# Kernel optimization log

Measured on AMD Instinct MI355X. Metric: run time of the kernel, lower is better.

The kernel has to match this reference:

```python
import jax, jax.numpy as jnp
import numpy as np

N, E = 100000, 1600000
D_IN, D_HID, D_OUT = 128, 64, 64
NEG_SLOPE = 0.2


def setup_inputs() -> dict:
    key = jax.random.key(0)
    ks = jax.random.split(key, 12)
    x = jax.random.normal(ks[0], (N, D_IN), dtype=jnp.float32)
    edge_index = jax.random.randint(ks[1], (2, E), 0, N, dtype=jnp.int64)
    edge_attr = jax.random.normal(ks[2], (E, 8), dtype=jnp.float32)
    s1 = 1.0 / np.sqrt(D_IN)
    s2 = 1.0 / np.sqrt(D_HID)
    return {
        "x": x,
        "edge_index": edge_index,
        "edge_attr": edge_attr,
        "W1": jax.random.normal(ks[3], (D_IN, D_HID), dtype=jnp.float32) * s1,
        "att_src1": jax.random.normal(ks[4], (D_HID,), dtype=jnp.float32) * s2,
        "att_dst1": jax.random.normal(ks[5], (D_HID,), dtype=jnp.float32) * s2,
        "b1": jnp.zeros((D_HID,), dtype=jnp.float32),
        "W2": jax.random.normal(ks[6], (D_HID, D_OUT), dtype=jnp.float32) * s2,
        "att_src2": jax.random.normal(ks[7], (D_OUT,), dtype=jnp.float32) * (1.0 / np.sqrt(D_OUT)),
        "att_dst2": jax.random.normal(ks[8], (D_OUT,), dtype=jnp.float32) * (1.0 / np.sqrt(D_OUT)),
        "b2": jnp.zeros((D_OUT,), dtype=jnp.float32),
    }


def gat_conv(x, src, dst, W, att_src, att_dst, b, n_nodes):
    # h = W x  (single head)
    h = x @ W                                   # [N, F]
    a_src = h @ att_src                         # [N]
    a_dst = h @ att_dst                         # [N]
    e = jax.nn.leaky_relu(a_src[src] + a_dst[dst], NEG_SLOPE)  # [E]
    # softmax over incoming edges per target node (numerically stable)
    e_max = jax.ops.segment_max(e, dst, num_segments=n_nodes)
    w = jnp.exp(e - e_max[dst])
    denom = jax.ops.segment_sum(w, dst, num_segments=n_nodes)
    alpha = w / (denom[dst] + 1e-16)            # [E]
    out = jax.ops.segment_sum(h[src] * alpha[:, None], dst, num_segments=n_nodes)
    return out + b


def reference(x, edge_index, edge_attr, W1, att_src1, att_dst1, b1, W2, att_src2, att_dst2, b2):
    n_nodes = x.shape[0]
    # PyG GATConv default: add self-loops; edge_attr unused (edge_dim=None)
    loops = jnp.arange(n_nodes, dtype=edge_index.dtype)
    src = jnp.concatenate([edge_index[0], loops])
    dst = jnp.concatenate([edge_index[1], loops])
    h = gat_conv(x, src, dst, W1, att_src1, att_dst1, b1, n_nodes)
    h = jax.nn.relu(h)
    h = gat_conv(h, src, dst, W2, att_src2, att_dst2, b2, n_nodes)
    # global_mean_pool with batch=None -> mean over all nodes, shape [1, D_OUT]
    return jnp.mean(h, axis=0, keepdims=True)
```

## Files before the change

### kernel.cpp

```cpp
#include <hip/hip_runtime.h>
#include <hip/hip_bf16.h>
#include <cstdint>

#define NEG_SLOPE 0.2f
#define SCAN_ELEMS 1024
#define BUCKET_SHIFT 9
#define CHUNK 2048

typedef __attribute__((ext_vector_type(4))) int            i32x4;
typedef __attribute__((ext_vector_type(4))) float          f32x4;
typedef __attribute__((ext_vector_type(8))) unsigned short u16x8;
typedef __attribute__((ext_vector_type(4))) unsigned short u16x4;

__device__ inline unsigned short f2bf(float f) {
    unsigned xi = __float_as_uint(f);
    unsigned r = xi + 0x7fffu + ((xi >> 16) & 1u);
    return (unsigned short)(r >> 16);
}
__device__ inline float bflo(unsigned g) { return __uint_as_float(g << 16); }
__device__ inline float bfhi(unsigned g) { return __uint_as_float(g & 0xffff0000u); }

__device__ inline int get_ei(const int* ei, int is64, long idx) {
    return is64 ? ei[2 * idx] : ei[(int)idx];
}

__device__ inline int detect_is64(const int* __restrict__ ei, int tid) {
    __shared__ int dred[4];
    int v = 0;
    for (int i = tid; i < 2048; i += 256) v |= ei[2 * i + 1];
#pragma unroll
    for (int off = 32; off; off >>= 1) v |= __shfl_xor(v, off);
    if ((tid & 63) == 0) dred[tid >> 6] = v;
    __syncthreads();
    int r = dred[0] | dred[1] | dred[2] | dred[3];
    __syncthreads();
    return (r == 0) ? 1 : 0;
}

__global__ __launch_bounds__(256) void p1_hist(const int* __restrict__ ei,
                                               int* __restrict__ HH,
                                               int E, int n, int nblk) {
    __shared__ int cnt[256];
    int tid = threadIdx.x;
    int is64 = detect_is64(ei, tid);
    int nbuk = (n + (1 << BUCKET_SHIFT) - 1) >> BUCKET_SHIFT;
    for (int b = tid; b < nbuk; b += 256) cnt[b] = 0;
    __syncthreads();
    int total = E + n;
    int beg = blockIdx.x * CHUNK;
    int end = beg + CHUNK; if (end > total) end = total;
    for (int i = beg + tid; i < end; i += 256) {
        int d = (i < E) ? get_ei(ei, is64, (long)E + i) : (i - E);
        atomicAdd(&cnt[d >> BUCKET_SHIFT], 1);
    }
    __syncthreads();
    for (int b = tid; b < nbuk; b += 256) HH[b * nblk + blockIdx.x] = cnt[b];
}

__global__ __launch_bounds__(256) void scan1_kernel(const int* __restrict__ src,
                                                    int* __restrict__ bsums, int n) {
    int t = threadIdx.x;
    int i0 = blockIdx.x * SCAN_ELEMS + 4 * t;
    int4 v = make_int4(0, 0, 0, 0);
    if (i0 + 3 < n) v = *(const int4*)(src + i0);
    else {
        if (i0 + 0 < n) v.x = src[i0 + 0];
        if (i0 + 1 < n) v.y = src[i0 + 1];
        if (i0 + 2 < n) v.z = src[i0 + 2];
        if (i0 + 3 < n) v.w = src[i0 + 3];
    }
    int s = v.x + v.y + v.z + v.w;
#pragma unroll
    for (int off = 32; off; off >>= 1) s += __shfl_down(s, off);
    __shared__ int ws[4];
    if ((t & 63) == 0) ws[t >> 6] = s;
    __syncthreads();
    if (t == 0) bsums[blockIdx.x] = ws[0] + ws[1] + ws[2] + ws[3];
}

__global__ __launch_bounds__(256) void scan3g_kernel(const int* __restrict__ src,
                                                     const int* __restrict__ bsums,
                                                     int* __restrict__ out, int n, int nb) {
    int b = blockIdx.x;
    int t = threadIdx.x;
    __shared__ int sb[256];
    int bv = (t < nb) ? bsums[t] : 0;
    sb[t] = bv;
    __syncthreads();
    for (int off = 1; off < 256; off <<= 1) {
        int u = (t >= off) ? sb[t - off] : 0;
        __syncthreads();
        sb[t] += u;
        __syncthreads();
    }
    int blockbase = (b == 0) ? 0 : sb[b - 1];

    int i0 = b * SCAN_ELEMS + 4 * t;
    int4 v = make_int4(0, 0, 0, 0);
    if (i0 + 3 < n) v = *(const int4*)(src + i0);
    else {
        if (i0 + 0 < n) v.x = src[i0 + 0];
        if (i0 + 1 < n) v.y = src[i0 + 1];
        if (i0 + 2 < n) v.z = src[i0 + 2];
        if (i0 + 3 < n) v.w = src[i0 + 3];
    }
    int s0 = v.x, s1 = s0 + v.y, s2 = s1 + v.z, s3 = s2 + v.w;
    __shared__ int sh[256];
    sh[t] = s3;
    __syncthreads();
    for (int off = 1; off < 256; off <<= 1) {
        int u = (t >= off) ? sh[t - off] : 0;
        __syncthreads();
        sh[t] += u;
        __syncthreads();
    }
    int base = blockbase + sh[t] - s3;
    if (i0 + 0 < n) out[i0 + 0] = base;
    if (i0 + 1 < n) out[i0 + 1] = base + s0;
    if (i0 + 2 < n) out[i0 + 2] = base + s1;
    if (i0 + 3 < n) out[i0 + 3] = base + s2;
}

__global__ __launch_bounds__(256) void p3_scatter(const int* __restrict__ ei,
                                                  const int* __restrict__ scanHH,
                                                  int* __restrict__ sorted,
                                                  int E, int n, int nblk) {
    __shared__ int base[256];
    __shared__ int cur[256];
    int tid = threadIdx.x;
    int is64 = detect_is64(ei, tid);
    int nbuk = (n + (1 << BUCKET_SHIFT) - 1) >> BUCKET_SHIFT;
    for (int b = tid; b < nbuk; b += 256) {
        base[b] = scanHH[b * nblk + blockIdx.x];
        cur[b] = 0;
    }
    __syncthreads();
    int total = E + n;
    int beg = blockIdx.x * CHUNK;
    int end = beg + CHUNK; if (end > total) end = total;
    for (int i = beg + tid; i < end; i += 256) {
        int s, d;
        if (i < E) {
            s = get_ei(ei, is64, i);
            d = get_ei(ei, is64, (long)E + i);
        } else {
            s = d = i - E;
        }
        int b = d >> BUCKET_SHIFT;
        int p = base[b] + atomicAdd(&cur[b], 1);
        sorted[p] = (s << BUCKET_SHIFT) | (d & ((1 << BUCKET_SHIFT) - 1));
    }
}

__global__ __launch_bounds__(256) void p4_finalize(const int* __restrict__ scanHH,
                                                   const int* __restrict__ sorted,
                                                   int* __restrict__ ptr,
                                                   int* __restrict__ csr_src,
                                                   int n, int nblk, int T) {
    int b = blockIdx.x;
    int nbuk = gridDim.x;
    int tid = threadIdx.x;
    int node0 = b << BUCKET_SHIFT;
    int nn = n - node0; if (nn > (1 << BUCKET_SHIFT)) nn = 1 << BUCKET_SHIFT;
    int beg = scanHH[b * nblk];
    int end = (b + 1 < nbuk) ? scanHH[(b + 1) * nblk] : T;

    __shared__ int cnt[512];
    __shared__ int pair[256];
    __shared__ int exc[512];
    cnt[tid] = 0; cnt[tid + 256] = 0;
    __syncthreads();
    for (int j = beg + tid; j < end; j += 256) {
        int v = sorted[j];
        atomicAdd(&cnt[v & ((1 << BUCKET_SHIFT) - 1)], 1);
    }
    __syncthreads();
    int psum = cnt[2 * tid] + cnt[2 * tid + 1];
    pair[tid] = psum;
    __syncthreads();
    for (int off = 1; off < 256; off <<= 1) {
        int u = (tid >= off) ? pair[tid - off] : 0;
        __syncthreads();
        pair[tid] += u;
        __syncthreads();
    }
    int pexc = pair[tid] - psum;
    exc[2 * tid] = pexc;
    exc[2 * tid + 1] = pexc + cnt[2 * tid];
    __syncthreads();
    for (int i = tid; i < nn; i += 256) ptr[node0 + i] = beg + exc[i];
    if (node0 + nn == n && tid == 0) ptr[n] = T;
    cnt[tid] = exc[tid]; cnt[tid + 256] = exc[tid + 256];
    __syncthreads();
    for (int j = beg + tid; j < end; j += 256) {
        int v = sorted[j];
        int p = beg + atomicAdd(&cnt[v & ((1 << BUCKET_SHIFT) - 1)], 1);
        csr_src[p] = ((unsigned)v) >> BUCKET_SHIFT;
    }
}

__global__ __launch_bounds__(256) void pack_w(const float* __restrict__ W1,
                                              const float* __restrict__ W2,
                                              unsigned short* __restrict__ wp1,
                                              unsigned short* __restrict__ wp2) {
    int t = blockIdx.x * 256 + threadIdx.x;
    if (t >= 24 * 64) return;
    int f = t >> 6, l = t & 63;
    int lm = l & 15, lg = l >> 4;
    const float* W = (f < 16) ? W1 : W2;
    unsigned short* wp = (f < 16) ? wp1 : wp2;
    int idx = (f < 16) ? f : (f - 16);
    int kt = idx >> 2, ct = idx & 3;
    union { u16x8 v; unsigned short u[8]; } o;
#pragma unroll
    for (int e = 0; e < 8; ++e)
        o.u[e] = f2bf(W[(size_t)(32 * kt + 8 * lg + e) * 64 + 16 * ct + lm]);
    *(u16x8*)(wp + ((size_t)idx * 64 + l) * 8) = o.v;
}

#define MFMA_BF16(acc, a, b) \
    asm("s_nop 1\n\tv_mfma_f32_16x16x32_bf16 %0, %1, %2, %0" \
        : "+v"(acc) : "v"(a), "v"(b))

template <int KT, bool XBF>
__global__ __launch_bounds__(256) void proj_mfma(const void* __restrict__ xin,
                                                 const unsigned short* __restrict__ Wp,
                                                 const float* __restrict__ att_s,
                                                 const float* __restrict__ att_d,
                                                 unsigned short* __restrict__ h2,
                                                 float* __restrict__ asrc,
                                                 float* __restrict__ adst, int n) {
    constexpr int K = 32 * KT;
    __shared__ alignas(16) unsigned short lb[4][16 * 72];
    int tid = threadIdx.x;
    int wid = tid >> 6, l = tid & 63;
    int lm = l & 15, lg = l >> 4;

    int node0 = blockIdx.x * 64 + wid * 16;
    if (node0 >= n) return;

    float as_c[4], ad_c[4];
#pragma unroll
    for (int ct = 0; ct < 4; ++ct) {
        as_c[ct] = att_s[16 * ct + lm];
        ad_c[ct] = att_d[16 * ct + lm];
    }

    f32x4 acc[4] = {};

    int arow = node0 + lm;
    bool rowok = arow < n;

#pragma unroll
    for (int kt = 0; kt < KT; ++kt) {
        i32x4 af = {0, 0, 0, 0};
        if (XBF) {
            const unsigned short* xb = (const unsigned short*)xin
                                       + (size_t)arow * K + 32 * kt + 8 * lg;
            if (rowok) af = *(const i32x4*)xb;
        } else {
            const float* xp = (const float*)xin + (size_t)arow * K + 8 * lg + 32 * kt;
            float4 v0 = make_float4(0.f, 0.f, 0.f, 0.f);
            float4 v1 = v0;
            if (rowok) {
                v0 = *(const float4*)(xp);
                v1 = *(const float4*)(xp + 4);
            }
            af[0] = (int)((unsigned)f2bf(v0.x) | ((unsigned)f2bf(v0.y) << 16));
            af[1] = (int)((unsigned)f2bf(v0.z) | ((unsigned)f2bf(v0.w) << 16));
            af[2] = (int)((unsigned)f2bf(v1.x) | ((unsigned)f2bf(v1.y) << 16));
            af[3] = (int)((unsigned)f2bf(v1.z) | ((unsigned)f2bf(v1.w) << 16));
        }
#pragma unroll
        for (int ct = 0; ct < 4; ++ct) {
            i32x4 bf = *(const i32x4*)(Wp + (((kt * 4 + ct) * 64) + l) * 8);
            MFMA_BF16(acc[ct], af, bf);
        }
    }
    asm volatile("s_nop 7\n\ts_nop 7"
                 : "+v"(acc[0]), "+v"(acc[1]), "+v"(acc[2]), "+v"(acc[3]));

    float ps[4], pd[4];
#pragma unroll
    for (int r = 0; r < 4; ++r) {
        float s = 0.f, d = 0.f;
#pragma unroll
        for (int ct = 0; ct < 4; ++ct) {
            s = fmaf(acc[ct][r], as_c[ct], s);
            d = fmaf(acc[ct][r], ad_c[ct], d);
        }
        ps[r] = s; pd[r] = d;
    }
#pragma unroll
    for (int off = 1; off < 16; off <<= 1) {
#pragma unroll
        for (int r = 0; r < 4; ++r) {
            ps[r] += __shfl_xor(ps[r], off);
            pd[r] += __shfl_xor(pd[r], off);
        }
    }
    if (lm == 0) {
#pragma unroll
        for (int r = 0; r < 4; ++r) {
            int node = node0 + 4 * lg + r;
            if (node < n) { asrc[node] = ps[r]; adst[node] = pd[r]; }
        }
    }

    unsigned short* wb = lb[wid];
#pragma unroll
    for (int ct = 0; ct < 4; ++ct)
#pragma unroll
        for (int r = 0; r < 4; ++r)
            wb[(4 * lg + r) * 72 + 16 * ct + lm] = f2bf(acc[ct][r]);
    asm volatile("s_waitcnt lgkmcnt(0)" ::: "memory");
    int ch = l & 7;
#pragma unroll
    for (int p = 0; p < 2; ++p) {
        int rr = (l >> 3) + 8 * p;
        u16x8 ov = *(const u16x8*)(wb + rr * 72 + 8 * ch);
        int onode = node0 + rr;
        if (onode < n)
            *(u16x8*)(h2 + (size_t)onode * 64 + 8 * ch) = ov;
    }
}

template <bool FMEAN>
__global__ __launch_bounds__(256) void agg_kernel(const int* __restrict__ ptr,
                                                  const int* __restrict__ srcs,
                                                  const unsigned short* __restrict__ h2,
                                                  const float* __restrict__ asrc,
                                                  const float* __restrict__ adst,
                                                  const float* __restrict__ bias,
                                                  unsigned short* __restrict__ outbf,
                                                  float* __restrict__ partials,
                                                  int n, int do_relu) {
    __shared__ int2  sm[4][64];
    __shared__ float red[256];
    int tid = threadIdx.x;
    int lane = tid & 63, wid = tid >> 6;
    int slot = lane >> 4, f = lane & 15;
    const char* h2b = (const char*)h2;
    unsigned fo = (unsigned)f << 3;
    float4 bv = *(const float4*)(bias + 4 * f);
    float ms0 = 0.f, ms1 = 0.f, ms2 = 0.f, ms3 = 0.f;

    int gwave = (blockIdx.x * blockDim.x + tid) >> 6;
    int nwaves = (gridDim.x * blockDim.x) >> 6;
    for (int node = gwave; node < n; node += nwaves) {
        int beg = ptr[node], end = ptr[node + 1];
        float ad = adst[node];
        float a0 = 0.f, a1 = 0.f, a2 = 0.f, a3 = 0.f, wsum = 0.f;
        for (int b = beg; b < end; b += 64) {
            int blen = end - b; if (blen > 64) blen = 64;
            int sv = 0; float wv = 0.f;
            if (lane < blen) {
                sv = srcs[b + lane];
                float e = asrc[sv] + ad;
                e = (e > 0.f) ? e : NEG_SLOPE * e;
                wv = __expf(e);
            }
            wsum += wv;
            sm[wid][lane] = make_int2(sv, __float_as_int(wv));
            int ni = (blen + 15) >> 4;
            for (int j = 0; j < ni; ++j) {
                int2 swv[4];
#pragma unroll
                for (int u = 0; u < 4; ++u)
                    swv[u] = sm[wid][16 * j + 4 * u + slot];
                uint2 g[4]; float w[4];
#pragma unroll
                for (int u = 0; u < 4; ++u) {
                    w[u] = __int_as_float(swv[u].y);
                    g[u] = *(const uint2*)(h2b + (((unsigned)swv[u].x << 7) + fo));
                }
#pragma unroll
                for (int u = 0; u < 4; ++u) {
                    a0 = fmaf(w[u], bflo(g[u].x), a0);
                    a1 = fmaf(w[u], bfhi(g[u].x), a1);
                    a2 = fmaf(w[u], bflo(g[u].y), a2);
                    a3 = fmaf(w[u], bfhi(g[u].y), a3);
                }
            }
        }
        a0 += __shfl_xor(a0, 16); a0 += __shfl_xor(a0, 32);
        a1 += __shfl_xor(a1, 16); a1 += __shfl_xor(a1, 32);
        a2 += __shfl_xor(a2, 16); a2 += __shfl_xor(a2, 32);
        a3 += __shfl_xor(a3, 16); a3 += __shfl_xor(a3, 32);
#pragma unroll
        for (int off = 32; off; off >>= 1) wsum += __shfl_xor(wsum, off);
        float inv = 1.f / (wsum + 1e-16f);
        float o0 = a0 * inv + bv.x;
        float o1 = a1 * inv + bv.y;
        float o2 = a2 * inv + bv.z;
        float o3 = a3 * inv + bv.w;
        if (!FMEAN) {
            if (do_relu) {
                o0 = fmaxf(o0, 0.f); o1 = fmaxf(o1, 0.f);
                o2 = fmaxf(o2, 0.f); o3 = fmaxf(o3, 0.f);
            }
            if (slot == 0) {
                u16x4 ov;
                ov[0] = f2bf(o0); ov[1] = f2bf(o1);
                ov[2] = f2bf(o2); ov[3] = f2bf(o3);
                *(u16x4*)(outbf + (size_t)node * 64 + 4 * f) = ov;
            }
        } else {
            if (slot == 0) { ms0 += o0; ms1 += o1; ms2 += o2; ms3 += o3; }
        }
    }
    if (FMEAN) {
        if (slot == 0)
            *(float4*)(red + wid * 64 + 4 * f) = make_float4(ms0, ms1, ms2, ms3);
        __syncthreads();
        if (tid < 64) {
            float t = red[tid] + red[64 + tid] + red[128 + tid] + red[192 + tid];
            partials[(size_t)blockIdx.x * 64 + tid] = t;
        }
    }
}

__global__ __launch_bounds__(256) void reduce_mean(const float* __restrict__ partials,
                                                   float* __restrict__ out,
                                                   int nb, float inv_n) {
    __shared__ float red[256];
    int f = threadIdx.x & 63;
    int w = threadIdx.x >> 6;
    int idx = blockIdx.x * 4 + w;
    int stride = gridDim.x * 4;
    float s = 0.f;
    for (int r = idx; r < nb; r += stride) s += partials[(size_t)r * 64 + f];
    red[threadIdx.x] = s;
    __syncthreads();
    if (w == 0) {
        float t = red[f] + red[64 + f] + red[128 + f] + red[192 + f];
        atomicAdd(&out[f], t * inv_n);
    }
}

extern "C" void kernel_launch(void* const* d_in, const int* in_sizes, int n_in,
                              void* d_out, int out_size, void* d_ws, size_t ws_size,
                              hipStream_t stream) {
    const float* x   = (const float*)d_in[0];
    const int*   ei  = (const int*)d_in[1];
    const float* W1  = (const float*)d_in[3];
    const float* as1 = (const float*)d_in[4];
    const float* ad1 = (const float*)d_in[5];
    const float* b1  = (const float*)d_in[6];
    const float* W2  = (const float*)d_in[7];
    const float* as2 = (const float*)d_in[8];
    const float* ad2 = (const float*)d_in[9];
    const float* b2  = (const float*)d_in[10];
    float* out = (float*)d_out;

    const int N = in_sizes[0] / 128;
    const int E = in_sizes[1] / 2;
    const int T = E + N;

    const int NBUK = (N + (1 << BUCKET_SHIFT) - 1) >> BUCKET_SHIFT;
    const int NBLK = (T + CHUNK - 1) / CHUNK;
    const int NHH  = NBUK * NBLK;
    const int NBS  = (NHH + SCAN_ELEMS - 1) / SCAN_ELEMS;
    const int AGRID = (N + 3) / 4;

    size_t off = 0;
    char* base = (char*)d_ws;
    auto alloc = [&](size_t bytes) -> void* {
        void* p = base + off;
        off += (bytes + 255) & ~(size_t)255;
        return p;
    };
    int*   ptr     = (int*)alloc(((size_t)N + 1) * 4);
    int*   bsums   = (int*)alloc(256 * 4);
    int*   HH      = (int*)alloc((size_t)NHH * 4);
    int*   scanHH  = (int*)alloc((size_t)NHH * 4);
    int*   csr_src = (int*)alloc((size_t)T * 4);
    float* asrc    = (float*)alloc((size_t)N * 4);
    float* adst    = (float*)alloc((size_t)N * 4);
    unsigned short* h2 = (unsigned short*)alloc((size_t)N * 64 * 2);
    unsigned short* bufB = (unsigned short*)alloc((size_t)N * 64 * 4);
    unsigned short* wp1 = (unsigned short*)alloc(16 * 64 * 8 * 2);
    unsigned short* wp2 = (unsigned short*)alloc(8 * 64 * 8 * 2);
    int*   sorted  = (int*)bufB;
    float* partials = (float*)bufB;
    (void)ws_size;

    pack_w<<<6, 256, 0, stream>>>(W1, W2, wp1, wp2);

    p1_hist<<<NBLK, 256, 0, stream>>>(ei, HH, E, N, NBLK);
    scan1_kernel<<<NBS, 256, 0, stream>>>(HH, bsums, NHH);
    scan3g_kernel<<<NBS, 256, 0, stream>>>(HH, bsums, scanHH, NHH, NBS);
    p3_scatter<<<NBLK, 256, 0, stream>>>(ei, scanHH, sorted, E, N, NBLK);
    p4_finalize<<<NBUK, 256, 0, stream>>>(scanHH, sorted, ptr, csr_src, N, NBLK, T);

    const int PGRID = (N + 63) / 64;

    proj_mfma<4, false><<<PGRID, 256, 0, stream>>>(x, wp1, as1, ad1, h2, asrc, adst, N);
    agg_kernel<false><<<AGRID, 256, 0, stream>>>(ptr, csr_src, h2, asrc, adst,
                                                 b1, bufB, nullptr, N, 1);

    proj_mfma<2, true><<<PGRID, 256, 0, stream>>>(bufB, wp2, as2, ad2, h2, asrc, adst, N);
    agg_kernel<true><<<AGRID, 256, 0, stream>>>(ptr, csr_src, h2, asrc, adst,
                                                b2, nullptr, partials, N, 0);
    hipMemsetAsync(out, 0, 64 * 4, stream);
    reduce_mean<<<64, 256, 0, stream>>>(partials, out, AGRID, 1.f / (float)N);
}
```

Baseline: 335.4 us.

## Restructure CSR build with global bucket counters and fuse histogram into projection

Replaces the per-block histogram matrix and two-pass scan with a single global bucket-count array filled by atomics. The histogram pass is fused into the first projection kernel. The scatter now stashes each chunk in LDS and reserves its bucket ranges with one atomic per bucket. It also doubles the gather unroll in aggregation, fixes the aggregation grid at 2048 blocks, and replaces the memset plus multi-block atomic reduction with a single-block reduction. Fewer launches and less scan work come at the cost of global atomic contention and a nondeterministic order within buckets.

```diff
diff --git a/kernel.cpp b/kernel.cpp
--- a/kernel.cpp
+++ b/kernel.cpp
@@ -3,9 +3,8 @@
 #include <cstdint>
 
 #define NEG_SLOPE 0.2f
-#define SCAN_ELEMS 1024
 #define BUCKET_SHIFT 9
-#define CHUNK 2048
+#define CHUNK 4096
 
 typedef __attribute__((ext_vector_type(4))) int            i32x4;
 typedef __attribute__((ext_vector_type(4))) float          f32x4;
@@ -37,185 +36,24 @@
     return (r == 0) ? 1 : 0;
 }
 
-__global__ __launch_bounds__(256) void p1_hist(const int* __restrict__ ei,
-                                               int* __restrict__ HH,
-                                               int E, int n, int nblk) {
+__device__ void p1_body(const int* __restrict__ ei, int* __restrict__ BT,
+                        int E, int n, int bid) {
     __shared__ int cnt[256];
     int tid = threadIdx.x;
     int is64 = detect_is64(ei, tid);
-    int nbuk = (n + (1 << BUCKET_SHIFT) - 1) >> BUCKET_SHIFT;
+    int nbuk = (n + 511) >> BUCKET_SHIFT;
     for (int b = tid; b < nbuk; b += 256) cnt[b] = 0;
     __syncthreads();
     int total = E + n;
-    int beg = blockIdx.x * CHUNK;
+    int beg = bid * CHUNK;
     int end = beg + CHUNK; if (end > total) end = total;
     for (int i = beg + tid; i < end; i += 256) {
         int d = (i < E) ? get_ei(ei, is64, (long)E + i) : (i - E);
         atomicAdd(&cnt[d >> BUCKET_SHIFT], 1);
     }
     __syncthreads();
-    for (int b = tid; b < nbuk; b += 256) HH[b * nblk + blockIdx.x] = cnt[b];
-}
-
-__global__ __launch_bounds__(256) void scan1_kernel(const int* __restrict__ src,
-                                                    int* __restrict__ bsums, int n) {
-    int t = threadIdx.x;
-    int i0 = blockIdx.x * SCAN_ELEMS + 4 * t;
-    int4 v = make_int4(0, 0, 0, 0);
-    if (i0 + 3 < n) v = *(const int4*)(src + i0);
-    else {
-        if (i0 + 0 < n) v.x = src[i0 + 0];
-        if (i0 + 1 < n) v.y = src[i0 + 1];
-        if (i0 + 2 < n) v.z = src[i0 + 2];
-        if (i0 + 3 < n) v.w = src[i0 + 3];
-    }
-    int s = v.x + v.y + v.z + v.w;
-#pragma unroll
-    for (int off = 32; off; off >>= 1) s += __shfl_down(s, off);
-    __shared__ int ws[4];
-    if ((t & 63) == 0) ws[t >> 6] = s;
-    __syncthreads();
-    if (t == 0) bsums[blockIdx.x] = ws[0] + ws[1] + ws[2] + ws[3];
-}
-
-__global__ __launch_bounds__(256) void scan3g_kernel(const int* __restrict__ src,
-                                                     const int* __restrict__ bsums,
-                                                     int* __restrict__ out, int n, int nb) {
-    int b = blockIdx.x;
-    int t = threadIdx.x;
-    __shared__ int sb[256];
-    int bv = (t < nb) ? bsums[t] : 0;
-    sb[t] = bv;
-    __syncthreads();
-    for (int off = 1; off < 256; off <<= 1) {
-        int u = (t >= off) ? sb[t - off] : 0;
-        __syncthreads();
-        sb[t] += u;
-        __syncthreads();
-    }
-    int blockbase = (b == 0) ? 0 : sb[b - 1];
-
-    int i0 = b * SCAN_ELEMS + 4 * t;
-    int4 v = make_int4(0, 0, 0, 0);
-    if (i0 + 3 < n) v = *(const int4*)(src + i0);
-    else {
-        if (i0 + 0 < n) v.x = src[i0 + 0];
-        if (i0 + 1 < n) v.y = src[i0 + 1];
-        if (i0 + 2 < n) v.z = src[i0 + 2];
-        if (i0 + 3 < n) v.w = src[i0 + 3];
-    }
-    int s0 = v.x, s1 = s0 + v.y, s2 = s1 + v.z, s3 = s2 + v.w;
-    __shared__ int sh[256];
-    sh[t] = s3;
-    __syncthreads();
-    for (int off = 1; off < 256; off <<= 1) {
-        int u = (t >= off) ? sh[t - off] : 0;
-        __syncthreads();
-        sh[t] += u;
-        __syncthreads();
-    }
-    int base = blockbase + sh[t] - s3;
-    if (i0 + 0 < n) out[i0 + 0] = base;
-    if (i0 + 1 < n) out[i0 + 1] = base + s0;
-    if (i0 + 2 < n) out[i0 + 2] = base + s1;
-    if (i0 + 3 < n) out[i0 + 3] = base + s2;
-}
-
-__global__ __launch_bounds__(256) void p3_scatter(const int* __restrict__ ei,
-                                                  const int* __restrict__ scanHH,
-                                                  int* __restrict__ sorted,
-                                                  int E, int n, int nblk) {
-    __shared__ int base[256];
-    __shared__ int cur[256];
-    int tid = threadIdx.x;
-    int is64 = detect_is64(ei, tid);
-    int nbuk = (n + (1 << BUCKET_SHIFT) - 1) >> BUCKET_SHIFT;
-    for (int b = tid; b < nbuk; b += 256) {
-        base[b] = scanHH[b * nblk + blockIdx.x];
-        cur[b] = 0;
-    }
-    __syncthreads();
-    int total = E + n;
-    int beg = blockIdx.x * CHUNK;
-    int end = beg + CHUNK; if (end > total) end = total;
-    for (int i = beg + tid; i < end; i += 256) {
-        int s, d;
-        if (i < E) {
-            s = get_ei(ei, is64, i);
-            d = get_ei(ei, is64, (long)E + i);
-        } else {
-            s = d = i - E;
-        }
-        int b = d >> BUCKET_SHIFT;
-        int p = base[b] + atomicAdd(&cur[b], 1);
-        sorted[p] = (s << BUCKET_SHIFT) | (d & ((1 << BUCKET_SHIFT) - 1));
-    }
-}
-
-__global__ __launch_bounds__(256) void p4_finalize(const int* __restrict__ scanHH,
-                                                   const int* __restrict__ sorted,
-                                                   int* __restrict__ ptr,
-                                                   int* __restrict__ csr_src,
-                                                   int n, int nblk, int T) {
-    int b = blockIdx.x;
-    int nbuk = gridDim.x;
-    int tid = threadIdx.x;
-    int node0 = b << BUCKET_SHIFT;
-    int nn = n - node0; if (nn > (1 << BUCKET_SHIFT)) nn = 1 << BUCKET_SHIFT;
-    int beg = scanHH[b * nblk];
-    int end = (b + 1 < nbuk) ? scanHH[(b + 1) * nblk] : T;
-
-    __shared__ int cnt[512];
-    __shared__ int pair[256];
-    __shared__ int exc[512];
-    cnt[tid] = 0; cnt[tid + 256] = 0;
-    __syncthreads();
-    for (int j = beg + tid; j < end; j += 256) {
-        int v = sorted[j];
-        atomicAdd(&cnt[v & ((1 << BUCKET_SHIFT) - 1)], 1);
-    }
-    __syncthreads();
-    int psum = cnt[2 * tid] + cnt[2 * tid + 1];
-    pair[tid] = psum;
-    __syncthreads();
-    for (int off = 1; off < 256; off <<= 1) {
-        int u = (tid >= off) ? pair[tid - off] : 0;
-        __syncthreads();
-        pair[tid] += u;
-        __syncthreads();
-    }
-    int pexc = pair[tid] - psum;
-    exc[2 * tid] = pexc;
-    exc[2 * tid + 1] = pexc + cnt[2 * tid];
-    __syncthreads();
-    for (int i = tid; i < nn; i += 256) ptr[node0 + i] = beg + exc[i];
-    if (node0 + nn == n && tid == 0) ptr[n] = T;
-    cnt[tid] = exc[tid]; cnt[tid + 256] = exc[tid + 256];
-    __syncthreads();
-    for (int j = beg + tid; j < end; j += 256) {
-        int v = sorted[j];
-        int p = beg + atomicAdd(&cnt[v & ((1 << BUCKET_SHIFT) - 1)], 1);
-        csr_src[p] = ((unsigned)v) >> BUCKET_SHIFT;
-    }
-}
-
-__global__ __launch_bounds__(256) void pack_w(const float* __restrict__ W1,
-                                              const float* __restrict__ W2,
-                                              unsigned short* __restrict__ wp1,
-                                              unsigned short* __restrict__ wp2) {
-    int t = blockIdx.x * 256 + threadIdx.x;
-    if (t >= 24 * 64) return;
-    int f = t >> 6, l = t & 63;
-    int lm = l & 15, lg = l >> 4;
-    const float* W = (f < 16) ? W1 : W2;
-    unsigned short* wp = (f < 16) ? wp1 : wp2;
-    int idx = (f < 16) ? f : (f - 16);
-    int kt = idx >> 2, ct = idx & 3;
-    union { u16x8 v; unsigned short u[8]; } o;
-#pragma unroll
-    for (int e = 0; e < 8; ++e)
-        o.u[e] = f2bf(W[(size_t)(32 * kt + 8 * lg + e) * 64 + 16 * ct + lm]);
-    *(u16x8*)(wp + ((size_t)idx * 64 + l) * 8) = o.v;
+    for (int b = tid; b < nbuk; b += 256)
+        if (cnt[b]) atomicAdd(&BT[b], cnt[b]);
 }
 
 #define MFMA_BF16(acc, a, b) \
@@ -223,20 +61,20 @@
         : "+v"(acc) : "v"(a), "v"(b))
 
 template <int KT, bool XBF>
-__global__ __launch_bounds__(256) void proj_mfma(const void* __restrict__ xin,
-                                                 const unsigned short* __restrict__ Wp,
-                                                 const float* __restrict__ att_s,
-                                                 const float* __restrict__ att_d,
-                                                 unsigned short* __restrict__ h2,
-                                                 float* __restrict__ asrc,
-                                                 float* __restrict__ adst, int n) {
+__device__ void proj_body(const void* __restrict__ xin,
+                          const unsigned short* __restrict__ Wp,
+                          const float* __restrict__ att_s,
+                          const float* __restrict__ att_d,
+                          unsigned short* __restrict__ h2,
+                          float* __restrict__ asrc,
+                          float* __restrict__ adst, int n, int bid) {
     constexpr int K = 32 * KT;
     __shared__ alignas(16) unsigned short lb[4][16 * 72];
     int tid = threadIdx.x;
     int wid = tid >> 6, l = tid & 63;
     int lm = l & 15, lg = l >> 4;
 
-    int node0 = blockIdx.x * 64 + wid * 16;
+    int node0 = bid * 64 + wid * 16;
     if (node0 >= n) return;
 
     float as_c[4], ad_c[4];
@@ -247,7 +85,6 @@
     }
 
     f32x4 acc[4] = {};
-
     int arow = node0 + lm;
     bool rowok = arow < n;
 
@@ -323,6 +160,163 @@
         if (onode < n)
             *(u16x8*)(h2 + (size_t)onode * 64 + 8 * ch) = ov;
     }
+}
+
+__global__ __launch_bounds__(256) void prep_kernel(const float* __restrict__ W1,
+                                                   const float* __restrict__ W2,
+                                                   unsigned short* __restrict__ wp1,
+                                                   unsigned short* __restrict__ wp2,
+                                                   int* __restrict__ BT, int nbuk) {
+    if (blockIdx.x == 6) {
+        for (int b = threadIdx.x; b < nbuk; b += 256) BT[b] = 0;
+        return;
+    }
+    int t = blockIdx.x * 256 + threadIdx.x;
+    int f = t >> 6, l = t & 63;
+    int lm = l & 15, lg = l >> 4;
+    const float* W = (f < 16) ? W1 : W2;
+    unsigned short* wp = (f < 16) ? wp1 : wp2;
+    int idx = (f < 16) ? f : (f - 16);
+    int kt = idx >> 2, ct = idx & 3;
+    union { u16x8 v; unsigned short u[8]; } o;
+#pragma unroll
+    for (int e = 0; e < 8; ++e)
+        o.u[e] = f2bf(W[(size_t)(32 * kt + 8 * lg + e) * 64 + 16 * ct + lm]);
+    *(u16x8*)(wp + ((size_t)idx * 64 + l) * 8) = o.v;
+}
+
+__global__ __launch_bounds__(256) void fused1(const float* __restrict__ x,
+                                              const unsigned short* __restrict__ wp1,
+                                              const float* __restrict__ as1,
+                                              const float* __restrict__ ad1,
+                                              unsigned short* __restrict__ h2,
+                                              float* __restrict__ asrc,
+                                              float* __restrict__ adst, int n,
+                                              const int* __restrict__ ei,
+                                              int* __restrict__ BT, int E, int pgrid) {
+    if ((int)blockIdx.x < pgrid)
+        proj_body<4, false>(x, wp1, as1, ad1, h2, asrc, adst, n, blockIdx.x);
+    else
+        p1_body(ei, BT, E, n, blockIdx.x - pgrid);
+}
+
+__global__ __launch_bounds__(256) void scan_bt(const int* __restrict__ BT,
+                                               int* __restrict__ BB,
+                                               int* __restrict__ cur, int nbuk) {
+    __shared__ int s[256];
+    int t = threadIdx.x;
+    int v = (t < nbuk) ? BT[t] : 0;
+    s[t] = v;
+    __syncthreads();
+    for (int off = 1; off < 256; off <<= 1) {
+        int u = (t >= off) ? s[t - off] : 0;
+        __syncthreads();
+        s[t] += u;
+        __syncthreads();
+    }
+    int exc = s[t] - v;
+    if (t < nbuk) { BB[t] = exc; cur[t] = exc; }
+    if (t == 0) BB[nbuk] = s[255];
+}
+
+__global__ __launch_bounds__(256) void p3_scatter(const int* __restrict__ ei,
+                                                  int* __restrict__ cur,
+                                                  int* __restrict__ sorted,
+                                                  int E, int n) {
+    __shared__ int stash[CHUNK];
+    __shared__ unsigned char stashB[CHUNK];
+    __shared__ int cnt[256];
+    __shared__ int base[256];
+    int tid = threadIdx.x;
+    int is64 = detect_is64(ei, tid);
+    int nbuk = (n + 511) >> BUCKET_SHIFT;
+    for (int b = tid; b < nbuk; b += 256) cnt[b] = 0;
+    __syncthreads();
+    int total = E + n;
+    int beg = blockIdx.x * CHUNK;
+    int end = beg + CHUNK; if (end > total) end = total;
+    for (int i = beg + tid; i < end; i += 256) {
+        int s, d;
+        if (i < E) {
+            s = get_ei(ei, is64, i);
+            d = get_ei(ei, is64, (long)E + i);
+        } else {
+            s = d = i - E;
+        }
+        int li = i - beg;
+        stash[li] = (s << BUCKET_SHIFT) | (d & 511);
+        stashB[li] = (unsigned char)(d >> BUCKET_SHIFT);
+        atomicAdd(&cnt[d >> BUCKET_SHIFT], 1);
+    }
+    __syncthreads();
+    for (int b = tid; b < nbuk; b += 256) {
+        int c = cnt[b];
+        base[b] = c ? atomicAdd(&cur[b], c) : 0;
+        cnt[b] = 0;
+    }
+    __syncthreads();
+    int cc = end - beg;
+    for (int li = tid; li < cc; li += 256) {
+        int b = stashB[li];
+        int p = base[b] + atomicAdd(&cnt[b], 1);
+        sorted[p] = stash[li];
+    }
+}
+
+__global__ __launch_bounds__(256) void p4_finalize(const int* __restrict__ BB,
+                                                   const int* __restrict__ sorted,
+                                                   int* __restrict__ ptr,
+                                                   int* __restrict__ csr_src,
+                                                   int n, int T) {
+    int b = blockIdx.x;
+    int tid = threadIdx.x;
+    int node0 = b << BUCKET_SHIFT;
+    int nn = n - node0; if (nn > 512) nn = 512;
+    int beg = BB[b];
+    int end = BB[b + 1];
+
+    __shared__ int cnt[512];
+    __shared__ int pair[256];
+    __shared__ int exc[512];
+    cnt[tid] = 0; cnt[tid + 256] = 0;
+    __syncthreads();
+    for (int j = beg + tid; j < end; j += 256) {
+        int v = sorted[j];
+        atomicAdd(&cnt[v & 511], 1);
+    }
+    __syncthreads();
+    int psum = cnt[2 * tid] + cnt[2 * tid + 1];
+    pair[tid] = psum;
+    __syncthreads();
+    for (int off = 1; off < 256; off <<= 1) {
+        int u = (tid >= off) ? pair[tid - off] : 0;
+        __syncthreads();
+        pair[tid] += u;
+        __syncthreads();
+    }
+    int pexc = pair[tid] - psum;
+    exc[2 * tid] = pexc;
+    exc[2 * tid + 1] = pexc + cnt[2 * tid];
+    __syncthreads();
+    for (int i = tid; i < nn; i += 256) ptr[node0 + i] = beg + exc[i];
+    if (node0 + nn == n && tid == 0) ptr[n] = T;
+    cnt[tid] = exc[tid]; cnt[tid + 256] = exc[tid + 256];
+    __syncthreads();
+    for (int j = beg + tid; j < end; j += 256) {
+        int v = sorted[j];
+        int p = beg + atomicAdd(&cnt[v & 511], 1);
+        csr_src[p] = ((unsigned)v) >> BUCKET_SHIFT;
+    }
+}
+
+__global__ __launch_bounds__(256) void proj2_kernel(const unsigned short* __restrict__ xin,
+                                                    const unsigned short* __restrict__ wp2,
+                                                    const float* __restrict__ as2,
+                                                    const float* __restrict__ ad2,
+                                                    unsigned short* __restrict__ h2,
+                                                    float* __restrict__ asrc,
+                                                    float* __restrict__ adst, int n) {
+    proj_body<2, true>(xin, wp2, as2, ad2, h2, asrc, adst, n, blockIdx.x);
 }
 
 template <bool FMEAN>
@@ -362,20 +356,20 @@
             }
             wsum += wv;
             sm[wid][lane] = make_int2(sv, __float_as_int(wv));
-            int ni = (blen + 15) >> 4;
+            int ni = (blen + 31) >> 5;
             for (int j = 0; j < ni; ++j) {
-                int2 swv[4];
-#pragma unroll
-                for (int u = 0; u < 4; ++u)
-                    swv[u] = sm[wid][16 * j + 4 * u + slot];
-                uint2 g[4]; float w[4];
-#pragma unroll
-                for (int u = 0; u < 4; ++u) {
+                int2 swv[8];
+#pragma unroll
+                for (int u = 0; u < 8; ++u)
+                    swv[u] = sm[wid][32 * j + 4 * u + slot];
+                uint2 g[8]; float w[8];
+#pragma unroll
+                for (int u = 0; u < 8; ++u) {
                     w[u] = __int_as_float(swv[u].y);
                     g[u] = *(const uint2*)(h2b + (((unsigned)swv[u].x << 7) + fo));
                 }
 #pragma unroll
-                for (int u = 0; u < 4; ++u) {
+                for (int u = 0; u < 8; ++u) {
                     a0 = fmaf(w[u], bflo(g[u].x), a0);
                     a1 = fmaf(w[u], bfhi(g[u].x), a1);
                     a2 = fmaf(w[u], bflo(g[u].y), a2);
@@ -420,22 +414,21 @@
     }
 }
 
-__global__ __launch_bounds__(256) void reduce_mean(const float* __restrict__ partials,
-                                                   float* __restrict__ out,
-                                                   int nb, float inv_n) {
-    __shared__ float red[256];
+__global__ __launch_bounds__(1024) void reduce_mean(const float* __restrict__ partials,
+                                                    float* __restrict__ out,
+                                                    int nb, float inv_n) {
+    __shared__ float red[1024];
     int f = threadIdx.x & 63;
     int w = threadIdx.x >> 6;
-    int idx = blockIdx.x * 4 + w;
-    int stride = gridDim.x * 4;
     float s = 0.f;
-    for (int r = idx; r < nb; r += stride) s += partials[(size_t)r * 64 + f];
+    for (int r = w; r < nb; r += 16) s += partials[(size_t)r * 64 + f];
     red[threadIdx.x] = s;
     __syncthreads();
-    if (w == 0) {
-        float t = red[f] + red[64 + f] + red[128 + f] + red[192 + f];
-        atomicAdd(&out[f], t * inv_n);
-    }
+    for (int step = 8; step >= 1; step >>= 1) {
+        if (w < step) red[w * 64 + f] += red[(w + step) * 64 + f];
+        __syncthreads();
+    }
+    if (w == 0) out[f] = red[f] * inv_n;
 }
 
 extern "C" void kernel_launch(void* const* d_in, const int* in_sizes, int n_in,
@@ -457,11 +450,10 @@
     const int E = in_sizes[1] / 2;
     const int T = E + N;
 
-    const int NBUK = (N + (1 << BUCKET_SHIFT) - 1) >> BUCKET_SHIFT;
-    const int NBLK = (T + CHUNK - 1) / CHUNK;
-    const int NHH  = NBUK * NBLK;
-    const int NBS  = (NHH + SCAN_ELEMS - 1) / SCAN_ELEMS;
-    const int AGRID = (N + 3) / 4;
+    const int NBUK  = (N + 511) >> BUCKET_SHIFT;
+    const int NBLK  = (T + CHUNK - 1) / CHUNK;
+    const int PGRID = (N + 63) / 64;
+    const int AGRID = 2048;
 
     size_t off = 0;
     char* base = (char*)d_ws;
@@ -471,9 +463,9 @@
         return p;
     };
     int*   ptr     = (int*)alloc(((size_t)N + 1) * 4);
-    int*   bsums   = (int*)alloc(256 * 4);
-    int*   HH      = (int*)alloc((size_t)NHH * 4);
-    int*   scanHH  = (int*)alloc((size_t)NHH * 4);
+    int*   BT      = (int*)alloc(256 * 4);
+    int*   BB      = (int*)alloc(257 * 4);
+    int*   cur     = (int*)alloc(256 * 4);
     int*   csr_src = (int*)alloc((size_t)T * 4);
     float* asrc    = (float*)alloc((size_t)N * 4);
     float* adst    = (float*)alloc((size_t)N * 4);
@@ -485,23 +477,16 @@
     float* partials = (float*)bufB;
     (void)ws_size;
 
-    pack_w<<<6, 256, 0, stream>>>(W1, W2, wp1, wp2);
-
-    p1_hist<<<NBLK, 256, 0, stream>>>(ei, HH, E, N, NBLK);
-    scan1_kernel<<<NBS, 256, 0, stream>>>(HH, bsums, NHH);
-    scan3g_kernel<<<NBS, 256, 0, stream>>>(HH, bsums, scanHH, NHH, NBS);
-    p3_scatter<<<NBLK, 256, 0, stream>>>(ei, scanHH, sorted, E, N, NBLK);
-    p4_finalize<<<NBUK, 256, 0, stream>>>(scanHH, sorted, ptr, csr_src, N, NBLK, T);
-
-    const int PGRID = (N + 63) / 64;
-
-    proj_mfma<4, false><<<PGRID, 256, 0, stream>>>(x, wp1, as1, ad1, h2, asrc, adst, N);
+    prep_kernel<<<7, 256, 0, stream>>>(W1, W2, wp1, wp2, BT, NBUK);
+    fused1<<<PGRID + NBLK, 256, 0, stream>>>(x, wp1, as1, ad1, h2, asrc, adst, N,
+                                             ei, BT, E, PGRID);
+    scan_bt<<<1, 256, 0, stream>>>(BT, BB, cur, NBUK);
+    p3_scatter<<<NBLK, 256, 0, stream>>>(ei, cur, sorted, E, N);
+    p4_finalize<<<NBUK, 256, 0, stream>>>(BB, sorted, ptr, csr_src, N, T);
     agg_kernel<false><<<AGRID, 256, 0, stream>>>(ptr, csr_src, h2, asrc, adst,
                                                  b1, bufB, nullptr, N, 1);
-
-    proj_mfma<2, true><<<PGRID, 256, 0, stream>>>(bufB, wp2, as2, ad2, h2, asrc, adst, N);
+    proj2_kernel<<<PGRID, 256, 0, stream>>>(bufB, wp2, as2, ad2, h2, asrc, adst, N);
     agg_kernel<true><<<AGRID, 256, 0, stream>>>(ptr, csr_src, h2, asrc, adst,
                                                 b2, nullptr, partials, N, 0);
-    hipMemsetAsync(out, 0, 64 * 4, stream);
-    reduce_mean<<<64, 256, 0, stream>>>(partials, out, AGRID, 1.f / (float)N);
-}
+    reduce_mean<<<1, 1024, 0, stream>>>(partials, out, AGRID, 1.f / (float)N);
+}
```

New measurement: 361.8 us. +7.9%, slower.
